# Kernel tuning notes

Measured on AMD Instinct MI355X. Metric: run time of the kernel, lower is better.

The kernel has to match this reference:

```python
import jax, jax.numpy as jnp
import numpy as np

N_NODES = 50000
N_EDGES = 800000
NFEAT, NHID, NCLASS = 128, 256, 64


def setup_inputs() -> dict:
    key = jax.random.key(0)
    ks = jax.random.split(key, 8)
    x = jax.random.normal(ks[0], (N_NODES, NFEAT), dtype=jnp.float32)
    edge_index = jax.random.randint(ks[1], (2, N_EDGES), 0, N_NODES, dtype=jnp.int64)
    s1 = 1.0 / np.sqrt(NFEAT)
    s2 = 1.0 / np.sqrt(NHID)
    W1_neigh = jax.random.normal(ks[2], (NFEAT, NHID), dtype=jnp.float32) * s1
    W1_root = jax.random.normal(ks[3], (NFEAT, NHID), dtype=jnp.float32) * s1
    b1 = jnp.zeros((NHID,), dtype=jnp.float32)
    W2_neigh = jax.random.normal(ks[4], (NHID, NCLASS), dtype=jnp.float32) * s2
    W2_root = jax.random.normal(ks[5], (NHID, NCLASS), dtype=jnp.float32) * s2
    b2 = jnp.zeros((NCLASS,), dtype=jnp.float32)
    return {"x": x, "edge_index": edge_index, "W1_neigh": W1_neigh,
            "W1_root": W1_root, "b1": b1, "W2_neigh": W2_neigh,
            "W2_root": W2_root, "b2": b2}


def _sage_conv(h, src, dst, n_nodes, W_neigh, W_root, b):
    # mean aggregation of source features into destination nodes
    msg = h[src]                                                   # [E, d]
    summed = jax.ops.segment_sum(msg, dst, num_segments=n_nodes)   # [N, d]
    cnt = jax.ops.segment_sum(jnp.ones((src.shape[0],), h.dtype), dst,
                              num_segments=n_nodes)                # [N]
    mean = summed / jnp.maximum(cnt, 1.0)[:, None]
    return mean @ W_neigh + h @ W_root + b


def reference(x, edge_index, W1_neigh, W1_root, b1, W2_neigh, W2_root, b2):
    src, dst = edge_index[0], edge_index[1]
    n = x.shape[0]
    h = jax.nn.relu(_sage_conv(x, src, dst, n, W1_neigh, W1_root, b1))
    # dropout is identity in eval mode
    out = _sage_conv(h, src, dst, n, W2_neigh, W2_root, b2)
    return out
```

## Files before the change

kernel.cpp:

```cpp
#include <hip/hip_runtime.h>

#define N_NODES 50000
#define N_EDGES 800000
#define NFEAT   128
#define NHID    256
#define NCLASS  64

#define ELLCAP  64

#define NBUCK   56
#define BWIDTH  896
#define BCAP    16384
#define BIN_CH  4096
#define BIN_B   ((N_EDGES + BIN_CH - 1) / BIN_CH)
#define NFINE   ((N_NODES + 127) / 128)
#define FPB     7

#define CVTX_B  ((N_NODES * 32 + 255) / 256)
#define CVTW_B  (((65536 + 32768) + 255) / 256)

typedef unsigned short u16;
typedef unsigned int   u32;
typedef __attribute__((ext_vector_type(8))) short s16x8;
typedef __attribute__((ext_vector_type(4))) float f32x4;

__device__ inline u16 f2bf(float f) {
    u32 u = __float_as_uint(f);
    u32 r = (u + 0x7FFFu + ((u >> 16) & 1u)) >> 16;
    return (u16)r;
}
__device__ inline float bflo(u32 v) { return __uint_as_float(v << 16); }
__device__ inline float bfhi(u32 v) { return __uint_as_float(v & 0xFFFF0000u); }

#define GLOAD_LDS16(g, l)                                                        \
    __builtin_amdgcn_global_load_lds(                                            \
        (const __attribute__((address_space(1))) u32*)(const void*)(g),          \
        (__attribute__((address_space(3))) u32*)(void*)(l), 16, 0, 0)

__global__ __launch_bounds__(256) void prep_kernel(const float* __restrict__ x,
                                                   const int* __restrict__ ei,
                                                   const float* __restrict__ W1r,
                                                   const float* __restrict__ W1n,
                                                   const float* __restrict__ W2n,
                                                   const float* __restrict__ W2r,
                                                   u16* __restrict__ xa,
                                                   u32* __restrict__ gcnt,
                                                   u32* __restrict__ bbuf,
                                                   u16* __restrict__ W1t,
                                                   u16* __restrict__ W2t) {
    int b = blockIdx.x;
    if (b < BIN_B) {
        __shared__ u32 hist[NBUCK];
        __shared__ u32 base[NBUCK];
        int tid = threadIdx.x;
        if (tid < NBUCK) hist[tid] = 0;
        __syncthreads();
        u32 ek[16]; u32 rk[16]; int bk[16];
        int i0 = b * BIN_CH;
        #pragma unroll
        for (int k = 0; k < 16; ++k) {
            int i = i0 + k * 256 + tid;
            bk[k] = -1;
            if (i < N_EDGES) {
                u32 s = (u32)ei[i];
                u32 d = (u32)ei[N_EDGES + i];
                int bu = (int)(d / BWIDTH);
                ek[k] = (d << 16) | s;
                bk[k] = bu;
                rk[k] = atomicAdd(&hist[bu], 1u);
            }
        }
        __syncthreads();
        if (tid < NBUCK) base[tid] = atomicAdd(&gcnt[tid], hist[tid]);
        __syncthreads();
        #pragma unroll
        for (int k = 0; k < 16; ++k) {
            if (bk[k] >= 0) {
                u32 pos = base[bk[k]] + rk[k];
                if (pos < BCAP) bbuf[((u32)bk[k] << 14) + pos] = ek[k];
            }
        }
    } else if (b < BIN_B + CVTX_B) {
        int idx = (b - BIN_B) * 256 + threadIdx.x;
        if (idx >= N_NODES * 32) return;
        int r  = idx >> 5;
        int c4 = (idx & 31) * 4;
        float4 v = *reinterpret_cast<const float4*>(x + (size_t)r * NFEAT + c4);
        uint2 o;
        o.x = (u32)f2bf(v.x) | ((u32)f2bf(v.y) << 16);
        o.y = (u32)f2bf(v.z) | ((u32)f2bf(v.w) << 16);
        *reinterpret_cast<uint2*>(xa + (size_t)r * 256 + c4) = o;
    } else {
        int id = (b - BIN_B - CVTX_B) * 256 + threadIdx.x;
        if (id < 65536) {
            int k = id & 255, n = id >> 8;
            float v = (k < NFEAT) ? W1r[(size_t)k * NHID + n]
                                  : W1n[(size_t)(k - NFEAT) * NHID + n];
            W1t[(size_t)n * 256 + k] = f2bf(v);
        } else if (id < 65536 + 32768) {
            int j = id - 65536;
            int k = j & 255, n = j >> 8;
            float v = (n < NCLASS) ? W2n[(size_t)k * NCLASS + n]
                                   : W2r[(size_t)k * NCLASS + (n - NCLASS)];
            W2t[(size_t)n * 256 + k] = f2bf(v);
        }
    }
}

__global__ __launch_bounds__(512) void ell_build_kernel(const u32* __restrict__ bbuf,
                                                        const u32* __restrict__ gcnt,
                                                        int* __restrict__ cnt,
                                                        u16* __restrict__ ell) {
    __shared__ u32 hist[128];
    int tid = threadIdx.x;
    int f   = blockIdx.x;
    int cb  = f / FPB;
    int n0  = f * 128;
    if (tid < 128) hist[tid] = 0;
    __syncthreads();
    int m = (int)gcnt[cb]; if (m > BCAP) m = BCAP;
    const u32* bk = bbuf + ((u32)cb << 14);
    int i = tid;
    for (; i + 1536 < m; i += 2048) {
        u32 e0 = bk[i], e1 = bk[i + 512], e2 = bk[i + 1024], e3 = bk[i + 1536];
        u32 d0 = (e0 >> 16) - (u32)n0, d1 = (e1 >> 16) - (u32)n0;
        u32 d2 = (e2 >> 16) - (u32)n0, d3 = (e3 >> 16) - (u32)n0;
        if (d0 < 128u) { u32 p = atomicAdd(&hist[d0], 1u); if (p < ELLCAP) ell[(size_t)(n0 + (int)d0) * ELLCAP + p] = (u16)e0; }
        if (d1 < 128u) { u32 p = atomicAdd(&hist[d1], 1u); if (p < ELLCAP) ell[(size_t)(n0 + (int)d1) * ELLCAP + p] = (u16)e1; }
        if (d2 < 128u) { u32 p = atomicAdd(&hist[d2], 1u); if (p < ELLCAP) ell[(size_t)(n0 + (int)d2) * ELLCAP + p] = (u16)e2; }
        if (d3 < 128u) { u32 p = atomicAdd(&hist[d3], 1u); if (p < ELLCAP) ell[(size_t)(n0 + (int)d3) * ELLCAP + p] = (u16)e3; }
    }
    for (; i < m; i += 512) {
        u32 e = bk[i];
        u32 d = (e >> 16) - (u32)n0;
        if (d < 128u) { u32 p = atomicAdd(&hist[d], 1u); if (p < ELLCAP) ell[(size_t)(n0 + (int)d) * ELLCAP + p] = (u16)e; }
    }
    __syncthreads();
    if (tid < 128) cnt[n0 + tid] = (int)hist[tid];
}

#define ACC8(v)                                                      \
    do { a[0] += bflo((v).x); a[1] += bfhi((v).x);                   \
         a[2] += bflo((v).y); a[3] += bfhi((v).y);                   \
         a[4] += bflo((v).z); a[5] += bfhi((v).z);                   \
         a[6] += bflo((v).w); a[7] += bfhi((v).w); } while (0)

__global__ __launch_bounds__(256) void gather1_kernel(const int* __restrict__ cnt,
                                                      const u16* __restrict__ ell,
                                                      u16* __restrict__ xa) {
    int gtid = blockIdx.x * 256 + threadIdx.x;
    int node = gtid >> 6;
    if (node >= N_NODES) return;
    int lane = threadIdx.x & 63;
    int g = lane >> 4, lr = lane & 15;
    const u32* xrow = reinterpret_cast<const u32*>(xa);
    const u16* idx = ell + (size_t)node * ELLCAP;
    int deg = cnt[node];
    if (deg > ELLCAP) deg = ELLCAP;
    float a[8] = {};
    int j = 0;
    for (; j + 16 <= deg; j += 16) {
        int s0 = idx[j + g], s1 = idx[j + 4 + g], s2 = idx[j + 8 + g], s3 = idx[j + 12 + g];
        uint4 v0 = *reinterpret_cast<const uint4*>(xrow + (size_t)s0 * 128 + lr * 4);
        uint4 v1 = *reinterpret_cast<const uint4*>(xrow + (size_t)s1 * 128 + lr * 4);
        uint4 v2 = *reinterpret_cast<const uint4*>(xrow + (size_t)s2 * 128 + lr * 4);
        uint4 v3 = *reinterpret_cast<const uint4*>(xrow + (size_t)s3 * 128 + lr * 4);
        ACC8(v0); ACC8(v1); ACC8(v2); ACC8(v3);
    }
    for (; j + 4 <= deg; j += 4) {
        int s0 = idx[j + g];
        uint4 v0 = *reinterpret_cast<const uint4*>(xrow + (size_t)s0 * 128 + lr * 4);
        ACC8(v0);
    }
    if (g < deg - j) {
        int s0 = idx[j + g];
        uint4 v0 = *reinterpret_cast<const uint4*>(xrow + (size_t)s0 * 128 + lr * 4);
        ACC8(v0);
    }
    #pragma unroll
    for (int k = 0; k < 8; ++k) {
        a[k] += __shfl_xor(a[k], 16);
        a[k] += __shfl_xor(a[k], 32);
    }
    if (g == 0) {
        float invd = 1.0f / fmaxf((float)deg, 1.0f);
        uint4 pk;
        pk.x = (u32)f2bf(a[0] * invd) | ((u32)f2bf(a[1] * invd) << 16);
        pk.y = (u32)f2bf(a[2] * invd) | ((u32)f2bf(a[3] * invd) << 16);
        pk.z = (u32)f2bf(a[4] * invd) | ((u32)f2bf(a[5] * invd) << 16);
        pk.w = (u32)f2bf(a[6] * invd) | ((u32)f2bf(a[7] * invd) << 16);
        *reinterpret_cast<uint4*>(reinterpret_cast<u32*>(xa) + (size_t)node * 128 + 64 + lr * 4) = pk;
    }
}

__global__ __launch_bounds__(256) void gather2_kernel(const int* __restrict__ cnt,
                                                      const u16* __restrict__ ell,
                                                      const u16* __restrict__ t,
                                                      float* __restrict__ out) {
    int gtid = blockIdx.x * 256 + threadIdx.x;
    int node = gtid >> 6;
    if (node >= N_NODES) return;
    int lane = threadIdx.x & 63;
    int g = lane >> 3, lr = lane & 7;
    const u32* trow = reinterpret_cast<const u32*>(t);
    const u16* idx = ell + (size_t)node * ELLCAP;
    int deg = cnt[node];
    if (deg > ELLCAP) deg = ELLCAP;
    float a[8] = {};
    int j = 0;
    for (; j + 16 <= deg; j += 16) {
        int s0 = idx[j + g], s1 = idx[j + 8 + g];
        uint4 v0 = *reinterpret_cast<const uint4*>(trow + (size_t)s0 * 32 + lr * 4);
        uint4 v1 = *reinterpret_cast<const uint4*>(trow + (size_t)s1 * 32 + lr * 4);
        ACC8(v0); ACC8(v1);
    }
    for (; j + 8 <= deg; j += 8) {
        int s0 = idx[j + g];
        uint4 v0 = *reinterpret_cast<const uint4*>(trow + (size_t)s0 * 32 + lr * 4);
        ACC8(v0);
    }
    if (g < deg - j) {
        int s0 = idx[j + g];
        uint4 v0 = *reinterpret_cast<const uint4*>(trow + (size_t)s0 * 32 + lr * 4);
        ACC8(v0);
    }
    #pragma unroll
    for (int k = 0; k < 8; ++k) {
        a[k] += __shfl_xor(a[k], 8);
        a[k] += __shfl_xor(a[k], 16);
        a[k] += __shfl_xor(a[k], 32);
    }
    if (g == 0) {
        float invd = 1.0f / fmaxf((float)deg, 1.0f);
        float* o = out + (size_t)node * NCLASS + lr * 8;
        float4 o0 = *reinterpret_cast<float4*>(o);
        float4 o1 = *reinterpret_cast<float4*>(o + 4);
        o0.x += a[0] * invd; o0.y += a[1] * invd; o0.z += a[2] * invd; o0.w += a[3] * invd;
        o1.x += a[4] * invd; o1.y += a[5] * invd; o1.z += a[6] * invd; o1.w += a[7] * invd;
        *reinterpret_cast<float4*>(o) = o0;
        *reinterpret_cast<float4*>(o + 4) = o1;
    }
}

__global__ __launch_bounds__(256) void gemm12_fused(const u16* __restrict__ xa,
                                                    const u16* __restrict__ W1t,
                                                    const float* __restrict__ b1,
                                                    const u16* __restrict__ W2t,
                                                    const float* __restrict__ b2,
                                                    u16* __restrict__ t,
                                                    float* __restrict__ out) {
    __shared__ u16 As[128 * 32];
    __shared__ u16 Bs[128 * 32];
    __shared__ u16 hs[128 * 256];
    const int tid = threadIdx.x;
    const int r0 = blockIdx.x * 128;
    const int wid = tid >> 6, ln = tid & 63;
    const int wm = (wid & 1) * 64, wn = (wid >> 1) * 64;
    const int lr = ln & 15;
    const int lq = ln >> 4;

    #pragma unroll 1
    for (int n0 = 0; n0 < 256; n0 += 128) {
        f32x4 acc[4][4] = {};
        for (int k0 = 0; k0 < 256; k0 += 32) {
            #pragma unroll
            for (int it = 0; it < 2; ++it) {
                int c   = it * 256 + tid;
                int row = c >> 2;
                int ko  = (c & 3) * 8;
                GLOAD_LDS16(xa  + (size_t)(r0 + row) * 256 + k0 + ko, As + c * 8);
                GLOAD_LDS16(W1t + (size_t)(n0 + row) * 256 + k0 + ko, Bs + c * 8);
            }
            __syncthreads();

            s16x8 af[4], bf[4];
            #pragma unroll
            for (int i = 0; i < 4; ++i)
                af[i] = *reinterpret_cast<const s16x8*>(As + (wm + i * 16 + lr) * 32 + lq * 8);
            #pragma unroll
            for (int j = 0; j < 4; ++j)
                bf[j] = *reinterpret_cast<const s16x8*>(Bs + (wn + j * 16 + lr) * 32 + lq * 8);
            #pragma unroll
            for (int i = 0; i < 4; ++i)
                #pragma unroll
                for (int j = 0; j < 4; ++j)
                    acc[i][j] = __builtin_amdgcn_mfma_f32_16x16x32_bf16(af[i], bf[j], acc[i][j], 0, 0, 0);
            __syncthreads();
        }
        #pragma unroll
        for (int i = 0; i < 4; ++i) {
            #pragma unroll
            for (int j = 0; j < 4; ++j) {
                int col = n0 + wn + j * 16 + lr;
                float bias = b1[col];
                #pragma unroll
                for (int r = 0; r < 4; ++r) {
                    int row = wm + i * 16 + lq * 4 + r;
                    hs[row * 256 + (col ^ ((row & 7) << 3))] =
                        f2bf(fmaxf(acc[i][j][r] + bias, 0.0f));
                }
            }
        }
    }

    f32x4 acc[4][4] = {};
    for (int k0 = 0; k0 < 256; k0 += 32) {
        {
            int c0 = tid, c1 = 256 + tid;
            GLOAD_LDS16(W2t + (size_t)(c0 >> 2) * 256 + k0 + (c0 & 3) * 8, Bs + c0 * 8);
            GLOAD_LDS16(W2t + (size_t)(c1 >> 2) * 256 + k0 + (c1 & 3) * 8, Bs + c1 * 8);
        }
        __syncthreads();

        s16x8 af[4], bf[4];
        #pragma unroll
        for (int i = 0; i < 4; ++i) {
            int row = wm + i * 16 + lr;
            af[i] = *reinterpret_cast<const s16x8*>(hs + row * 256 + ((k0 + lq * 8) ^ ((row & 7) << 3)));
        }
        #pragma unroll
        for (int j = 0; j < 4; ++j)
            bf[j] = *reinterpret_cast<const s16x8*>(Bs + (wn + j * 16 + lr) * 32 + lq * 8);
        #pragma unroll
        for (int i = 0; i < 4; ++i)
            #pragma unroll
            for (int j = 0; j < 4; ++j)
                acc[i][j] = __builtin_amdgcn_mfma_f32_16x16x32_bf16(af[i], bf[j], acc[i][j], 0, 0, 0);
        __syncthreads();
    }

    #pragma unroll
    for (int i = 0; i < 4; ++i) {
        #pragma unroll
        for (int j = 0; j < 4; ++j) {
            int col = wn + j * 16 + lr;
            #pragma unroll
            for (int r = 0; r < 4; ++r) {
                int row = r0 + wm + i * 16 + lq * 4 + r;
                if (row >= N_NODES) continue;
                if (col < NCLASS) {
                    t[(size_t)row * NCLASS + col] = f2bf(acc[i][j][r]);
                } else {
                    int c = col - NCLASS;
                    out[(size_t)row * NCLASS + c] = acc[i][j][r] + b2[c];
                }
            }
        }
    }
}

extern "C" void kernel_launch(void* const* d_in, const int* in_sizes, int n_in,
                              void* d_out, int out_size, void* d_ws, size_t ws_size,
                              hipStream_t stream) {
    const float* x    = (const float*)d_in[0];
    const int*   ei   = (const int*)d_in[1];
    const float* W1n  = (const float*)d_in[2];
    const float* W1r  = (const float*)d_in[3];
    const float* b1   = (const float*)d_in[4];
    const float* W2n  = (const float*)d_in[5];
    const float* W2r  = (const float*)d_in[6];
    const float* b2   = (const float*)d_in[7];
    float* out = (float*)d_out;

    u32* gcnt = (u32*)d_ws;
    u32* bbuf = gcnt + 64;
    int* cnt  = (int*)(bbuf + ((size_t)NBUCK << 14));
    u16* ell  = (u16*)(cnt + 50048);
    u16* xa   = ell + (size_t)N_NODES * ELLCAP;
    u16* t    = xa + (size_t)50048 * 256;
    u16* W1t  = t  + (size_t)N_NODES * 64;
    u16* W2t  = W1t + 65536;

    hipMemsetAsync(gcnt, 0, 64 * sizeof(u32), stream);

    prep_kernel<<<BIN_B + CVTX_B + CVTW_B, 256, 0, stream>>>(
        x, ei, W1r, W1n, W2n, W2r, xa, gcnt, bbuf, W1t, W2t);
    ell_build_kernel<<<NFINE, 512, 0, stream>>>(bbuf, gcnt, cnt, ell);

    gather1_kernel<<<(N_NODES * 64 + 255) / 256, 256, 0, stream>>>(cnt, ell, xa);

    gemm12_fused<<<NFINE, 256, 0, stream>>>(xa, W1t, b1, W2t, b2, t, out);

    gather2_kernel<<<(N_NODES * 64 + 255) / 256, 256, 0, stream>>>(cnt, ell, t, out);
}
```

Measured before the change: 191.7 us.

## Restructure fused GEMM: 64-row tiles, resident A tile, double-buffered weight loads

The fused two-layer GEMM now handles 64 rows per block instead of 128, which doubles the grid. It loads the block's full 256-wide input tile into swizzled LDS once and walks both layer-1 column halves and layer 2 in a single 24-step loop. Each step prefetches the next weight slice into a second LDS buffer while computing on the current one. The goal is to hide global load latency, drop one barrier per step and improve occupancy, at the cost of reloading the weights for twice as many blocks.

```diff
diff --git a/kernel.cpp b/kernel.cpp
--- a/kernel.cpp
+++ b/kernel.cpp
@@ -14,6 +14,7 @@
 #define BIN_CH  4096
 #define BIN_B   ((N_EDGES + BIN_CH - 1) / BIN_CH)
 #define NFINE   ((N_NODES + 127) / 128)
+#define NFINE2  ((N_NODES + 63) / 64)
 #define FPB     7
 
 #define CVTX_B  ((N_NODES * 32 + 255) / 256)
@@ -249,88 +250,88 @@
                                                     const float* __restrict__ b2,
                                                     u16* __restrict__ t,
                                                     float* __restrict__ out) {
-    __shared__ u16 As[128 * 32];
-    __shared__ u16 Bs[128 * 32];
-    __shared__ u16 hs[128 * 256];
+    __shared__ u16 Af[64 * 256];
+    __shared__ u16 Bs[2][128 * 32];
+    __shared__ u16 hs[64 * 256];
     const int tid = threadIdx.x;
-    const int r0 = blockIdx.x * 128;
+    const int r0 = blockIdx.x * 64;
     const int wid = tid >> 6, ln = tid & 63;
-    const int wm = (wid & 1) * 64, wn = (wid >> 1) * 64;
+    const int wm = (wid & 1) * 32, wn = (wid >> 1) * 64;
     const int lr = ln & 15;
     const int lq = ln >> 4;
 
+    #pragma unroll
+    for (int p = 0; p < 8; ++p) {
+        int c    = p * 256 + tid;
+        int row  = c >> 5;
+        int col8 = (c & 31) ^ (row & 7);
+        GLOAD_LDS16(xa + (size_t)(r0 + row) * 256 + col8 * 8, Af + c * 8);
+    }
+    #pragma unroll
+    for (int it = 0; it < 2; ++it) {
+        int c = it * 256 + tid;
+        GLOAD_LDS16(W1t + (size_t)(c >> 2) * 256 + (c & 3) * 8, &Bs[0][0] + c * 8);
+    }
+    __syncthreads();
+
+    f32x4 acc[2][4] = {};
+    int cur = 0;
     #pragma unroll 1
-    for (int n0 = 0; n0 < 256; n0 += 128) {
-        f32x4 acc[4][4] = {};
-        for (int k0 = 0; k0 < 256; k0 += 32) {
+    for (int s = 0; s < 24; ++s) {
+        if (s < 23) {
+            int sn = s + 1;
+            const u16* bsrc = (sn < 8) ? W1t : (sn < 16) ? (W1t + 128 * 256) : W2t;
+            int k0n = (sn & 7) * 32;
             #pragma unroll
             for (int it = 0; it < 2; ++it) {
-                int c   = it * 256 + tid;
-                int row = c >> 2;
-                int ko  = (c & 3) * 8;
-                GLOAD_LDS16(xa  + (size_t)(r0 + row) * 256 + k0 + ko, As + c * 8);
-                GLOAD_LDS16(W1t + (size_t)(n0 + row) * 256 + k0 + ko, Bs + c * 8);
-            }
-            __syncthreads();
-
-            s16x8 af[4], bf[4];
-            #pragma unroll
-            for (int i = 0; i < 4; ++i)
-                af[i] = *reinterpret_cast<const s16x8*>(As + (wm + i * 16 + lr) * 32 + lq * 8);
-            #pragma unroll
-            for (int j = 0; j < 4; ++j)
-                bf[j] = *reinterpret_cast<const s16x8*>(Bs + (wn + j * 16 + lr) * 32 + lq * 8);
-            #pragma unroll
-            for (int i = 0; i < 4; ++i)
-                #pragma unroll
-                for (int j = 0; j < 4; ++j)
-                    acc[i][j] = __builtin_amdgcn_mfma_f32_16x16x32_bf16(af[i], bf[j], acc[i][j], 0, 0, 0);
-            __syncthreads();
-        }
-        #pragma unroll
-        for (int i = 0; i < 4; ++i) {
-            #pragma unroll
-            for (int j = 0; j < 4; ++j) {
-                int col = n0 + wn + j * 16 + lr;
-                float bias = b1[col];
-                #pragma unroll
-                for (int r = 0; r < 4; ++r) {
-                    int row = wm + i * 16 + lq * 4 + r;
-                    hs[row * 256 + (col ^ ((row & 7) << 3))] =
-                        f2bf(fmaxf(acc[i][j][r] + bias, 0.0f));
-                }
-            }
-        }
-    }
-
-    f32x4 acc[4][4] = {};
-    for (int k0 = 0; k0 < 256; k0 += 32) {
-        {
-            int c0 = tid, c1 = 256 + tid;
-            GLOAD_LDS16(W2t + (size_t)(c0 >> 2) * 256 + k0 + (c0 & 3) * 8, Bs + c0 * 8);
-            GLOAD_LDS16(W2t + (size_t)(c1 >> 2) * 256 + k0 + (c1 & 3) * 8, Bs + c1 * 8);
-        }
-        __syncthreads();
-
-        s16x8 af[4], bf[4];
-        #pragma unroll
-        for (int i = 0; i < 4; ++i) {
+                int c = it * 256 + tid;
+                GLOAD_LDS16(bsrc + (size_t)(c >> 2) * 256 + k0n + (c & 3) * 8,
+                            &Bs[cur ^ 1][0] + c * 8);
+            }
+        }
+
+        int k0 = (s & 7) * 32;
+        const u16* asrc = (s < 16) ? Af : hs;
+        s16x8 af[2], bf[4];
+        #pragma unroll
+        for (int i = 0; i < 2; ++i) {
             int row = wm + i * 16 + lr;
-            af[i] = *reinterpret_cast<const s16x8*>(hs + row * 256 + ((k0 + lq * 8) ^ ((row & 7) << 3)));
+            af[i] = *reinterpret_cast<const s16x8*>(
+                asrc + row * 256 + ((k0 + lq * 8) ^ ((row & 7) << 3)));
         }
         #pragma unroll
         for (int j = 0; j < 4; ++j)
-            bf[j] = *reinterpret_cast<const s16x8*>(Bs + (wn + j * 16 + lr) * 32 + lq * 8);
-        #pragma unroll
-        for (int i = 0; i < 4; ++i)
+            bf[j] = *reinterpret_cast<const s16x8*>(&Bs[cur][0] + (wn + j * 16 + lr) * 32 + lq * 8);
+        #pragma unroll
+        for (int i = 0; i < 2; ++i)
             #pragma unroll
             for (int j = 0; j < 4; ++j)
                 acc[i][j] = __builtin_amdgcn_mfma_f32_16x16x32_bf16(af[i], bf[j], acc[i][j], 0, 0, 0);
+
+        if (s == 7 || s == 15) {
+            int half = s >> 3;
+            #pragma unroll
+            for (int i = 0; i < 2; ++i) {
+                #pragma unroll
+                for (int j = 0; j < 4; ++j) {
+                    int col = half * 128 + wn + j * 16 + lr;
+                    float bias = b1[col];
+                    #pragma unroll
+                    for (int r = 0; r < 4; ++r) {
+                        int row = wm + i * 16 + lq * 4 + r;
+                        hs[row * 256 + (col ^ ((row & 7) << 3))] =
+                            f2bf(fmaxf(acc[i][j][r] + bias, 0.0f));
+                        acc[i][j][r] = 0.0f;
+                    }
+                }
+            }
+        }
         __syncthreads();
-    }
-
-    #pragma unroll
-    for (int i = 0; i < 4; ++i) {
+        cur ^= 1;
+    }
+
+    #pragma unroll
+    for (int i = 0; i < 2; ++i) {
         #pragma unroll
         for (int j = 0; j < 4; ++j) {
             int col = wn + j * 16 + lr;
@@ -379,7 +380,7 @@
 
     gather1_kernel<<<(N_NODES * 64 + 255) / 256, 256, 0, stream>>>(cnt, ell, xa);
 
-    gemm12_fused<<<NFINE, 256, 0, stream>>>(xa, W1t, b1, W2t, b2, t, out);
+    gemm12_fused<<<NFINE2, 256, 0, stream>>>(xa, W1t, b1, W2t, b2, t, out);
 
     gather2_kernel<<<(N_NODES * 64 + 255) / 256, 256, 0, stream>>>(cnt, ell, t, out);
 }
```

Result: slower. 206.0 us (+7.5%).

## Shrink fused GEMM tile to 64 rows and load operands directly from global

Applied to the files above, without the earlier changes.

The fused two-layer GEMM now processes 64 rows per block instead of 128. Each wave covers a 64-column slice of the hidden layer and reads A and B fragments straight from global memory into registers, with no LDS staging and no per-k-step barriers. Only the hidden tile stays in LDS, at half the previous size, and launch bounds ask for 3 blocks per CU. This is meant to raise occupancy, double the block count and remove barrier stalls, at the cost of redundant global/L2 reads of xa and weights across waves and uncoalesced fragment loads.

```diff
diff --git a/kernel.cpp b/kernel.cpp
--- a/kernel.cpp
+++ b/kernel.cpp
@@ -14,6 +14,7 @@
 #define BIN_CH  4096
 #define BIN_B   ((N_EDGES + BIN_CH - 1) / BIN_CH)
 #define NFINE   ((N_NODES + 127) / 128)
+#define NFINE2  ((N_NODES + 63) / 64)
 #define FPB     7
 
 #define CVTX_B  ((N_NODES * 32 + 255) / 256)
@@ -242,101 +243,90 @@
     }
 }
 
-__global__ __launch_bounds__(256) void gemm12_fused(const u16* __restrict__ xa,
-                                                    const u16* __restrict__ W1t,
-                                                    const float* __restrict__ b1,
-                                                    const u16* __restrict__ W2t,
-                                                    const float* __restrict__ b2,
-                                                    u16* __restrict__ t,
-                                                    float* __restrict__ out) {
-    __shared__ u16 As[128 * 32];
-    __shared__ u16 Bs[128 * 32];
-    __shared__ u16 hs[128 * 256];
+__global__ __launch_bounds__(256, 3) void gemm12_fused(const u16* __restrict__ xa,
+                                                       const u16* __restrict__ W1t,
+                                                       const float* __restrict__ b1,
+                                                       const u16* __restrict__ W2t,
+                                                       const float* __restrict__ b2,
+                                                       u16* __restrict__ t,
+                                                       float* __restrict__ out) {
+    __shared__ u16 hs[64 * 256];
     const int tid = threadIdx.x;
-    const int r0 = blockIdx.x * 128;
+    const int r0 = blockIdx.x * 64;
     const int wid = tid >> 6, ln = tid & 63;
-    const int wm = (wid & 1) * 64, wn = (wid >> 1) * 64;
     const int lr = ln & 15;
     const int lq = ln >> 4;
 
-    #pragma unroll 1
-    for (int n0 = 0; n0 < 256; n0 += 128) {
+    const int wn1 = wid * 64;
+    {
         f32x4 acc[4][4] = {};
-        for (int k0 = 0; k0 < 256; k0 += 32) {
-            #pragma unroll
-            for (int it = 0; it < 2; ++it) {
-                int c   = it * 256 + tid;
-                int row = c >> 2;
-                int ko  = (c & 3) * 8;
-                GLOAD_LDS16(xa  + (size_t)(r0 + row) * 256 + k0 + ko, As + c * 8);
-                GLOAD_LDS16(W1t + (size_t)(n0 + row) * 256 + k0 + ko, Bs + c * 8);
-            }
-            __syncthreads();
-
+        #pragma unroll
+        for (int ks = 0; ks < 8; ++ks) {
+            const int k0 = ks * 32;
             s16x8 af[4], bf[4];
             #pragma unroll
             for (int i = 0; i < 4; ++i)
-                af[i] = *reinterpret_cast<const s16x8*>(As + (wm + i * 16 + lr) * 32 + lq * 8);
+                af[i] = *reinterpret_cast<const s16x8*>(
+                    xa + (size_t)(r0 + i * 16 + lr) * 256 + k0 + lq * 8);
             #pragma unroll
             for (int j = 0; j < 4; ++j)
-                bf[j] = *reinterpret_cast<const s16x8*>(Bs + (wn + j * 16 + lr) * 32 + lq * 8);
+                bf[j] = *reinterpret_cast<const s16x8*>(
+                    W1t + (size_t)(wn1 + j * 16 + lr) * 256 + k0 + lq * 8);
             #pragma unroll
             for (int i = 0; i < 4; ++i)
                 #pragma unroll
                 for (int j = 0; j < 4; ++j)
-                    acc[i][j] = __builtin_amdgcn_mfma_f32_16x16x32_bf16(af[i], bf[j], acc[i][j], 0, 0, 0);
-            __syncthreads();
-        }
-        #pragma unroll
-        for (int i = 0; i < 4; ++i) {
-            #pragma unroll
-            for (int j = 0; j < 4; ++j) {
-                int col = n0 + wn + j * 16 + lr;
-                float bias = b1[col];
+                    acc[i][j] = __builtin_amdgcn_mfma_f32_16x16x32_bf16(
+                        af[i], bf[j], acc[i][j], 0, 0, 0);
+        }
+        #pragma unroll
+        for (int j = 0; j < 4; ++j) {
+            int col = wn1 + j * 16 + lr;
+            float bias = b1[col];
+            #pragma unroll
+            for (int i = 0; i < 4; ++i)
                 #pragma unroll
                 for (int r = 0; r < 4; ++r) {
-                    int row = wm + i * 16 + lq * 4 + r;
+                    int row = i * 16 + lq * 4 + r;
                     hs[row * 256 + (col ^ ((row & 7) << 3))] =
                         f2bf(fmaxf(acc[i][j][r] + bias, 0.0f));
                 }
-            }
-        }
-    }
-
-    f32x4 acc[4][4] = {};
-    for (int k0 = 0; k0 < 256; k0 += 32) {
-        {
-            int c0 = tid, c1 = 256 + tid;
-            GLOAD_LDS16(W2t + (size_t)(c0 >> 2) * 256 + k0 + (c0 & 3) * 8, Bs + c0 * 8);
-            GLOAD_LDS16(W2t + (size_t)(c1 >> 2) * 256 + k0 + (c1 & 3) * 8, Bs + c1 * 8);
-        }
-        __syncthreads();
-
-        s16x8 af[4], bf[4];
+        }
+    }
+    __syncthreads();
+
+    const int wn2 = wid * 32;
+    f32x4 acc[4][2] = {};
+    #pragma unroll
+    for (int ks = 0; ks < 8; ++ks) {
+        const int k0 = ks * 32;
+        s16x8 af[4], bf[2];
         #pragma unroll
         for (int i = 0; i < 4; ++i) {
-            int row = wm + i * 16 + lr;
-            af[i] = *reinterpret_cast<const s16x8*>(hs + row * 256 + ((k0 + lq * 8) ^ ((row & 7) << 3)));
-        }
-        #pragma unroll
-        for (int j = 0; j < 4; ++j)
-            bf[j] = *reinterpret_cast<const s16x8*>(Bs + (wn + j * 16 + lr) * 32 + lq * 8);
+            int row = i * 16 + lr;
+            af[i] = *reinterpret_cast<const s16x8*>(
+                hs + row * 256 + ((k0 + lq * 8) ^ ((row & 7) << 3)));
+        }
+        #pragma unroll
+        for (int j = 0; j < 2; ++j)
+            bf[j] = *reinterpret_cast<const s16x8*>(
+                W2t + (size_t)(wn2 + j * 16 + lr) * 256 + k0 + lq * 8);
         #pragma unroll
         for (int i = 0; i < 4; ++i)
             #pragma unroll
-            for (int j = 0; j < 4; ++j)
-                acc[i][j] = __builtin_amdgcn_mfma_f32_16x16x32_bf16(af[i], bf[j], acc[i][j], 0, 0, 0);
-        __syncthreads();
+            for (int j = 0; j < 2; ++j)
+                acc[i][j] = __builtin_amdgcn_mfma_f32_16x16x32_bf16(
+                    af[i], bf[j], acc[i][j], 0, 0, 0);
     }
 
     #pragma unroll
     for (int i = 0; i < 4; ++i) {
         #pragma unroll
-        for (int j = 0; j < 4; ++j) {
-            int col = wn + j * 16 + lr;
+        for (int j = 0; j < 2; ++j) {
+            int col = wn2 + j * 16 + lr;
             #pragma unroll
             for (int r = 0; r < 4; ++r) {
-                int row = r0 + wm + i * 16 + lq * 4 + r;
+                int row = r0 + i * 16 + lq * 4 + r;
                 if (row >= N_NODES) continue;
                 if (col < NCLASS) {
                     t[(size_t)row * NCLASS + col] = f2bf(acc[i][j][r]);
@@ -379,7 +369,7 @@
 
     gather1_kernel<<<(N_NODES * 64 + 255) / 256, 256, 0, stream>>>(cnt, ell, xa);
 
-    gemm12_fused<<<NFINE, 256, 0, stream>>>(xa, W1t, b1, W2t, b2, t, out);
+    gemm12_fused<<<NFINE2, 256, 0, stream>>>(xa, W1t, b1, W2t, b2, t, out);
 
     gather2_kernel<<<(N_NODES * 64 + 255) / 256, 256, 0, stream>>>(cnt, ell, t, out);
 }
```

Result: slower. 201.5 us (+5.1%).
